# Kernel tuning notes

Hardware: AMD Instinct MI355X
Metric: run time of the kernel (lower is better)

## Reference

```python
import jax, jax.numpy as jnp
import numpy as np

N = 100000          # nodes
D_TEXT = 200        # text embedding dim
D_SEL = 2           # selector embedding dim (zero-padded in pos embs)
D = D_TEXT + D_SEL  # 202
E_TYPES = 6         # 3 forward edge types * 2 (backward edges)
M = 200000          # edges per edge type
N_POS = 512
SMALL_NUMBER = 1e-8


def position_embeddings(n_pos, demb, dpad):
    # Faithful to ProGraML PositionEmbeddings: sinusoid sin||cos, zero-padded.
    pos = jnp.arange(n_pos, dtype=jnp.float32)
    inv_freq = 1.0 / (10000.0 ** (jnp.arange(0, demb, 2, dtype=jnp.float32) / demb))
    sin_inp = pos[:, None] * inv_freq[None, :]                    # [n_pos, demb/2]
    emb = jnp.concatenate([jnp.sin(sin_inp), jnp.cos(sin_inp)], axis=-1)
    return jnp.concatenate([emb, jnp.zeros((n_pos, dpad), emb.dtype)], axis=1)  # [n_pos, demb+dpad]


def setup_inputs() -> dict:
    key = jax.random.key(0)
    ks = jax.random.split(key, 6)
    return {
        "node_states": jax.random.normal(ks[0], (N, D), jnp.float32),
        "edges": jax.random.randint(ks[1], (E_TYPES, M, 2), 0, N),      # [:, :, 0]=src, [:, :, 1]=tgt
        "pos_lists": jax.random.randint(ks[2], (E_TYPES, M), 0, N_POS),
        "W_transform": jax.random.normal(ks[3], (D, D * E_TYPES), jnp.float32) * 0.05,
        "b_transform": jnp.zeros((D * E_TYPES,), jnp.float32),
        "W_pos": jax.random.normal(ks[4], (D, D), jnp.float32) * 0.05,
        "b_pos": jnp.zeros((D,), jnp.float32),
    }


def reference(node_states, edges, pos_lists, W_transform, b_transform, W_pos, b_pos):
    # Positional gating: 2*sigmoid(Linear(position_embs))  -> [512, D]
    pos_embs = position_embeddings(N_POS, D_TEXT, D_SEL)
    pos_gating = 2.0 * jax.nn.sigmoid(pos_embs @ W_pos + b_pos)

    # Dense transform: [N, D] @ [D, E*D] -> view as [N, E, D]
    # (matches torch transpose(0,1).view(E, D, N) followed by per-type transpose back)
    prop = (node_states @ W_transform + b_transform).reshape(N, E_TYPES, D)

    src = edges[..., 0]  # [E, M]
    tgt = edges[..., 1]  # [E, M]

    # Per-edge-type gather of transformed source states: msgs[e, m] = prop[src[e, m], e]
    msgs = prop[src, jnp.arange(E_TYPES)[:, None], :]             # [E, M, D]
    msgs = msgs * pos_gating[pos_lists]                           # positional gate

    # Scatter-add over targets (all edge types fused into one segment_sum)
    flat_tgt = tgt.reshape(-1)
    summed = jax.ops.segment_sum(msgs.reshape(-1, D), flat_tgt, num_segments=N)  # [N, D]

    # Mean aggregation: bincount of targets, zeros treated as 1
    bincount = jax.ops.segment_sum(jnp.ones((E_TYPES * M,), jnp.float32), flat_tgt, num_segments=N)
    divisor = jnp.where(bincount == 0, 1.0, bincount) + SMALL_NUMBER
    return summed / divisor[:, None]
```

## Files before the change

### kernel.cpp

```cpp
#include <hip/hip_runtime.h>
#include <hip/hip_bf16.h>
#include <hip/hip_fp16.h>
#include <math.h>

#define NN   100000
#define NNP  100096
#define DD   202
#define ET   6
#define MM   200000
#define NE   (ET*MM)
#define NPOS 512
#define GDP  204
#define DE   1212
#define PDE  1216
#define KK   202
#define KP   224
#define NP   1280

typedef __attribute__((ext_vector_type(8))) short bf16x8;
typedef __attribute__((ext_vector_type(4))) float f32x4;

static __device__ inline unsigned short f2b(float f) {
    union { __hip_bfloat16 h; unsigned short s; } u;
    u.h = __float2bfloat16(f);
    return u.s;
}

static __device__ inline void glds16(const unsigned short* g, unsigned short* l) {
    __builtin_amdgcn_global_load_lds(
        (const __attribute__((address_space(1))) unsigned int*)g,
        (__attribute__((address_space(3))) unsigned int*)l, 16, 0, 0);
}

__global__ void gating_kernel(const float* __restrict__ W_pos,
                              const float* __restrict__ b_pos,
                              unsigned short* __restrict__ gat) {
    int p = blockIdx.x;
    __shared__ float emb[DD];
    int t = threadIdx.x;
    if (t < 100) {
        float invf = expf(-((float)t / 100.0f) * 9.210340371976184f);
        float si = (float)p * invf;
        emb[t]       = sinf(si);
        emb[100 + t] = cosf(si);
    } else if (t < 102) {
        emb[100 + t] = 0.0f;
    }
    __syncthreads();
    if (t < GDP) {
        float g = 0.0f;
        if (t < DD) {
            float acc = b_pos[t];
            for (int k = 0; k < DD; ++k) acc += emb[k] * W_pos[k * DD + t];
            g = 2.0f / (1.0f + expf(-acc));
        }
        union { __half h; unsigned short s; } u;
        u.h = __float2half_rn(g);
        gat[p * GDP + t] = u.s;
    }
}

__global__ void convB_kernel(const float* __restrict__ W, unsigned short* __restrict__ Bt) {
    int id = blockIdx.x * 256 + threadIdx.x;
    if (id >= NP * KP) return;
    int n = id / KP, k = id % KP;
    float v = (k < KK && n < DE) ? W[(size_t)k * DE + n] : 0.0f;
    Bt[id] = f2b(v);
}

__global__ void convA_kernel(const float* __restrict__ A, unsigned short* __restrict__ Abf) {
    int id = blockIdx.x * 256 + threadIdx.x;
    if (id >= NNP * (KP / 2)) return;
    int row = id / (KP / 2), kp = (id % (KP / 2)) * 2;
    float2 v = make_float2(0.0f, 0.0f);
    if (row < NN && kp < KK) v = *(const float2*)&A[(size_t)row * KK + kp];
    ushort2 o; o.x = f2b(v.x); o.y = f2b(v.y);
    *(ushort2*)&Abf[(size_t)row * KP + kp] = o;
}

__global__ __launch_bounds__(256) void gemm_mfma(const unsigned short* __restrict__ Abf,
                                                 const unsigned short* __restrict__ Bt,
                                                 const float* __restrict__ bias,
                                                 unsigned short* __restrict__ C) {
    __shared__ unsigned short lds[16384];
    unsigned short* sA = lds;
    unsigned short* sB = lds + 8192;
    unsigned short* sE = lds;

    int t    = threadIdx.x;
    int lane = t & 63;
    int wave = t >> 6;
    int q    = lane >> 4;
    int r16  = lane & 15;
    int wm   = (wave >> 1) * 64;
    int wn   = (wave & 1) * 64;
    int row0 = blockIdx.y * 128;
    int col0 = blockIdx.x * 128;

    int lrow = lane >> 2;
    int gch  = (lane & 3) ^ ((lrow >> 1) & 3);
    const unsigned short* aS0 = Abf + (size_t)(row0 + wave * 32 + lrow) * KP + gch * 8;
    const unsigned short* aS1 = aS0 + 16 * KP;
    const unsigned short* bS0 = Bt  + (size_t)(col0 + wave * 32 + lrow) * KP + gch * 8;
    const unsigned short* bS1 = bS0 + 16 * KP;

#define STAGE(b, kc) do {                                   \
        glds16(aS0 + (kc), &sA[(b)*4096 + wave*1024]);      \
        glds16(aS1 + (kc), &sA[(b)*4096 + wave*1024+512]);  \
        glds16(bS0 + (kc), &sB[(b)*4096 + wave*1024]);      \
        glds16(bS1 + (kc), &sB[(b)*4096 + wave*1024+512]);  \
    } while (0)

    f32x4 acc[4][4] = {};
    int swzr = (r16 >> 1) & 3;

    STAGE(0, 0);
    for (int k = 0; k < 7; ++k) {
        int cur = k & 1;
        if (k < 6) {
            STAGE(cur ^ 1, (k + 1) * 32);
            asm volatile("s_waitcnt vmcnt(4)" ::: "memory");
        } else {
            asm volatile("s_waitcnt vmcnt(0)" ::: "memory");
        }
        __builtin_amdgcn_s_barrier();

        bf16x8 a[4], b[4];
        int sbase = cur * 4096;
        #pragma unroll
        for (int mi = 0; mi < 4; ++mi)
            a[mi] = *(const bf16x8*)&sA[sbase + (wm + mi * 16 + r16) * 32 + (q ^ swzr) * 8];
        #pragma unroll
        for (int ni = 0; ni < 4; ++ni)
            b[ni] = *(const bf16x8*)&sB[sbase + (wn + ni * 16 + r16) * 32 + (q ^ swzr) * 8];
        #pragma unroll
        for (int mi = 0; mi < 4; ++mi)
            #pragma unroll
            for (int ni = 0; ni < 4; ++ni)
                acc[mi][ni] = __builtin_amdgcn_mfma_f32_16x16x32_bf16(a[mi], b[ni], acc[mi][ni], 0, 0, 0);

        __builtin_amdgcn_s_barrier();
    }
#undef STAGE

    float bb[4];
    #pragma unroll
    for (int ni = 0; ni < 4; ++ni) {
        int col = col0 + wn + ni * 16 + r16;
        bb[ni] = (col < DE) ? bias[col] : 0.0f;
    }
    int epi = wave * 1152;
    int rl = lane >> 3, ck = lane & 7;
    #pragma unroll
    for (int mi = 0; mi < 4; ++mi) {
        #pragma unroll
        for (int ni = 0; ni < 4; ++ni)
            #pragma unroll
            for (int ri = 0; ri < 4; ++ri)
                sE[epi + (q * 4 + ri) * 72 + ni * 16 + r16] = f2b(acc[mi][ni][ri] + bb[ni]);
        #pragma unroll
        for (int ii = 0; ii < 2; ++ii) {
            int rr = ii * 8 + rl;
            bf16x8 v = *(const bf16x8*)&sE[epi + rr * 72 + ck * 8];
            int grow = row0 + wm + mi * 16 + rr;
            int gcol = col0 + wn + ck * 8;
            if (grow < NN && gcol < PDE)
                *(bf16x8*)&C[(size_t)grow * PDE + gcol] = v;
        }
    }
}

__global__ __launch_bounds__(256) void count_kernel(const int* __restrict__ edges,
                                                    int* __restrict__ count) {
    int i = blockIdx.x * 256 + threadIdx.x;
    if (i >= NE) return;
    atomicAdd(&count[edges[2 * i + 1]], 1);
}

__global__ __launch_bounds__(256) void alloc_kernel(const int* __restrict__ count,
                                                    int* __restrict__ start,
                                                    int* __restrict__ cursor) {
    int t = blockIdx.x * 256 + threadIdx.x;
    int c = (t < NN) ? count[t] : 0;
    __shared__ int s[256];
    __shared__ int base;
    s[threadIdx.x] = c;
    __syncthreads();
    int v = c;
    for (int off = 1; off < 256; off <<= 1) {
        int u = (threadIdx.x >= off) ? s[threadIdx.x - off] : 0;
        __syncthreads();
        v += u;
        s[threadIdx.x] = v;
        __syncthreads();
    }
    if (threadIdx.x == 255) base = atomicAdd(cursor, v);
    __syncthreads();
    if (t < NN) start[t] = base + v - c;
}

__global__ __launch_bounds__(256) void scatter_kernel(const int* __restrict__ edges,
                                                      const int* __restrict__ pos_lists,
                                                      int* __restrict__ start,
                                                      unsigned* __restrict__ recs) {
    int i = blockIdx.x * 256 + threadIdx.x;
    if (i >= NE) return;
    int2 st = *(const int2*)&edges[2 * i];
    int e = (int)((unsigned)i / MM);
    unsigned rec = (unsigned)st.x | ((unsigned)e << 17) | ((unsigned)pos_lists[i] << 20);
    int p = atomicAdd(&start[st.y], 1);
    recs[p] = rec;
}

__global__ __launch_bounds__(256) void gather_kernel(const unsigned short* __restrict__ prop,
                                                     const unsigned short* __restrict__ gat,
                                                     const int* __restrict__ count,
                                                     const int* __restrict__ seg_end,
                                                     const unsigned* __restrict__ recs,
                                                     float* __restrict__ out) {
    int wid = blockIdx.x * 4 + (threadIdx.x >> 6);
    if (wid >= NN) return;
    int lane = threadIdx.x & 63;
    int c = count[wid];
    int end = seg_end[wid];
    int begin = end - c;
    int d = lane * 4;
    bool act = d < DD;
    float a0 = 0.f, a1 = 0.f, a2 = 0.f, a3 = 0.f;

    for (int base = begin; base < end; base += 64) {
        int n = end - base; if (n > 64) n = 64;
        unsigned rec = 0u;
        if (lane < n) rec = recs[base + lane];
        int poff = (int)(rec & 0x1FFFFu) * PDE + (int)((rec >> 17) & 7u) * DD;
        int goff = (int)(rec >> 20) * GDP;

        for (int jj = 0; jj < n; jj += 4) {
            int po[4], go[4];
            #pragma unroll
            for (int u = 0; u < 4; ++u) {
                int j = jj + u; if (j >= n) j = jj;
                po[u] = __shfl(poff, j);
                go[u] = __shfl(goff, j);
            }
            uint2 pv[4], gv[4];
            #pragma unroll
            for (int u = 0; u < 4; ++u) {
                pv[u] = make_uint2(0u, 0u);
                gv[u] = make_uint2(0u, 0u);
                if (act) {
                    pv[u] = *(const uint2*)&prop[po[u] + d];
                    gv[u] = *(const uint2*)&gat[go[u] + d];
                }
            }
            #pragma unroll
            for (int u = 0; u < 4; ++u) {
                if (jj + u < n || u == 0) {
                    float2 g01 = __half22float2(*(const __half2*)&gv[u].x);
                    float2 g23 = __half22float2(*(const __half2*)&gv[u].y);
                    a0 += __uint_as_float(pv[u].x << 16)         * g01.x;
                    a1 += __uint_as_float(pv[u].x & 0xffff0000u) * g01.y;
                    a2 += __uint_as_float(pv[u].y << 16)         * g23.x;
                    a3 += __uint_as_float(pv[u].y & 0xffff0000u) * g23.y;
                }
            }
        }
    }

    float div = (c == 0 ? 1.0f : (float)c) + 1e-8f;
    float inv = 1.0f / div;
    if (act) {
        float* orow = out + (size_t)wid * DD;
        *(float2*)&orow[d] = make_float2(a0 * inv, a1 * inv);
        if (d + 2 < DD) *(float2*)&orow[d + 2] = make_float2(a2 * inv, a3 * inv);
    }
}

extern "C" void kernel_launch(void* const* d_in, const int* in_sizes, int n_in,
                              void* d_out, int out_size, void* d_ws, size_t ws_size,
                              hipStream_t stream) {
    const float* node_states = (const float*)d_in[0];
    const int*   edges       = (const int*)d_in[1];
    const int*   pos_lists   = (const int*)d_in[2];
    const float* W_transform = (const float*)d_in[3];
    const float* b_transform = (const float*)d_in[4];
    const float* W_pos       = (const float*)d_in[5];
    const float* b_pos       = (const float*)d_in[6];
    float* out = (float*)d_out;

    char* ws = (char*)d_ws;
    unsigned short* gat = (unsigned short*)ws;  ws += (size_t)NPOS * GDP * 2;
    int* count  = (int*)ws;                     ws += (size_t)NN * 4;
    int* start  = (int*)ws;                     ws += (size_t)NN * 4;
    int* cursor = (int*)ws;                     ws += 16;
    unsigned short* Bt  = (unsigned short*)ws;  ws += (size_t)NP * KP * 2;
    unsigned short* Abf = (unsigned short*)ws;  ws += (size_t)NNP * KP * 2;
    unsigned* recs = (unsigned*)ws;             ws += (size_t)NE * 4;
    unsigned short* prop = (unsigned short*)ws;

    hipMemsetAsync(count, 0, NN * sizeof(int), stream);
    hipMemsetAsync(cursor, 0, sizeof(int), stream);

    gating_kernel<<<NPOS, 256, 0, stream>>>(W_pos, b_pos, gat);
    convB_kernel<<<(NP * KP + 255) / 256, 256, 0, stream>>>(W_transform, Bt);
    convA_kernel<<<(NNP * (KP / 2) + 255) / 256, 256, 0, stream>>>(node_states, Abf);

    dim3 g2(NP / 128, NNP / 128);
    gemm_mfma<<<g2, 256, 0, stream>>>(Abf, Bt, b_transform, prop);

    count_kernel<<<(NE + 255) / 256, 256, 0, stream>>>(edges, count);
    alloc_kernel<<<(NN + 255) / 256, 256, 0, stream>>>(count, start, cursor);
    scatter_kernel<<<(NE + 255) / 256, 256, 0, stream>>>(edges, pos_lists, start, recs);
    gather_kernel<<<(NN + 3) / 4, 256, 0, stream>>>(prop, gat, count, start, recs, out);
}
```

Baseline: 631.8 us.

## Fuse prep kernels and GEMM with edge scatter into interleaved grids

```diff
diff --git a/kernel.cpp b/kernel.cpp
--- a/kernel.cpp
+++ b/kernel.cpp
@@ -17,6 +17,11 @@
 #define KP   224
 #define NP   1280
 
+#define NB_CONVB 1120
+#define NB_CA    10948
+#define PREPG    1564
+#define MAING    1564
+
 typedef __attribute__((ext_vector_type(8))) short bf16x8;
 typedef __attribute__((ext_vector_type(4))) float f32x4;
 
@@ -32,149 +37,80 @@
         (__attribute__((address_space(3))) unsigned int*)l, 16, 0, 0);
 }
 
-__global__ void gating_kernel(const float* __restrict__ W_pos,
-                              const float* __restrict__ b_pos,
-                              unsigned short* __restrict__ gat) {
-    int p = blockIdx.x;
+__global__ __launch_bounds__(256) void fused_prep(const float* __restrict__ W_pos,
+                                                  const float* __restrict__ b_pos,
+                                                  unsigned short* __restrict__ gat,
+                                                  const float* __restrict__ W,
+                                                  unsigned short* __restrict__ Bt,
+                                                  const float* __restrict__ A,
+                                                  unsigned short* __restrict__ Abf,
+                                                  const int* __restrict__ edges,
+                                                  int* __restrict__ count) {
     __shared__ float emb[DD];
+    int bid = blockIdx.x;
     int t = threadIdx.x;
-    if (t < 100) {
-        float invf = expf(-((float)t / 100.0f) * 9.210340371976184f);
-        float si = (float)p * invf;
-        emb[t]       = sinf(si);
-        emb[100 + t] = cosf(si);
-    } else if (t < 102) {
-        emb[100 + t] = 0.0f;
-    }
-    __syncthreads();
-    if (t < GDP) {
-        float g = 0.0f;
-        if (t < DD) {
-            float acc = b_pos[t];
-            for (int k = 0; k < DD; ++k) acc += emb[k] * W_pos[k * DD + t];
-            g = 2.0f / (1.0f + expf(-acc));
-        }
-        union { __half h; unsigned short s; } u;
-        u.h = __float2half_rn(g);
-        gat[p * GDP + t] = u.s;
-    }
-}
-
-__global__ void convB_kernel(const float* __restrict__ W, unsigned short* __restrict__ Bt) {
-    int id = blockIdx.x * 256 + threadIdx.x;
-    if (id >= NP * KP) return;
-    int n = id / KP, k = id % KP;
-    float v = (k < KK && n < DE) ? W[(size_t)k * DE + n] : 0.0f;
-    Bt[id] = f2b(v);
-}
-
-__global__ void convA_kernel(const float* __restrict__ A, unsigned short* __restrict__ Abf) {
-    int id = blockIdx.x * 256 + threadIdx.x;
-    if (id >= NNP * (KP / 2)) return;
-    int row = id / (KP / 2), kp = (id % (KP / 2)) * 2;
-    float2 v = make_float2(0.0f, 0.0f);
-    if (row < NN && kp < KK) v = *(const float2*)&A[(size_t)row * KK + kp];
-    ushort2 o; o.x = f2b(v.x); o.y = f2b(v.y);
-    *(ushort2*)&Abf[(size_t)row * KP + kp] = o;
-}
-
-__global__ __launch_bounds__(256) void gemm_mfma(const unsigned short* __restrict__ Abf,
-                                                 const unsigned short* __restrict__ Bt,
-                                                 const float* __restrict__ bias,
-                                                 unsigned short* __restrict__ C) {
-    __shared__ unsigned short lds[16384];
-    unsigned short* sA = lds;
-    unsigned short* sB = lds + 8192;
-    unsigned short* sE = lds;
-
-    int t    = threadIdx.x;
-    int lane = t & 63;
-    int wave = t >> 6;
-    int q    = lane >> 4;
-    int r16  = lane & 15;
-    int wm   = (wave >> 1) * 64;
-    int wn   = (wave & 1) * 64;
-    int row0 = blockIdx.y * 128;
-    int col0 = blockIdx.x * 128;
-
-    int lrow = lane >> 2;
-    int gch  = (lane & 3) ^ ((lrow >> 1) & 3);
-    const unsigned short* aS0 = Abf + (size_t)(row0 + wave * 32 + lrow) * KP + gch * 8;
-    const unsigned short* aS1 = aS0 + 16 * KP;
-    const unsigned short* bS0 = Bt  + (size_t)(col0 + wave * 32 + lrow) * KP + gch * 8;
-    const unsigned short* bS1 = bS0 + 16 * KP;
-
-#define STAGE(b, kc) do {                                   \
-        glds16(aS0 + (kc), &sA[(b)*4096 + wave*1024]);      \
-        glds16(aS1 + (kc), &sA[(b)*4096 + wave*1024+512]);  \
-        glds16(bS0 + (kc), &sB[(b)*4096 + wave*1024]);      \
-        glds16(bS1 + (kc), &sB[(b)*4096 + wave*1024+512]);  \
-    } while (0)
-
-    f32x4 acc[4][4] = {};
-    int swzr = (r16 >> 1) & 3;
-
-    STAGE(0, 0);
-    for (int k = 0; k < 7; ++k) {
-        int cur = k & 1;
-        if (k < 6) {
-            STAGE(cur ^ 1, (k + 1) * 32);
-            asm volatile("s_waitcnt vmcnt(4)" ::: "memory");
-        } else {
-            asm volatile("s_waitcnt vmcnt(0)" ::: "memory");
-        }
-        __builtin_amdgcn_s_barrier();
-
-        bf16x8 a[4], b[4];
-        int sbase = cur * 4096;
-        #pragma unroll
-        for (int mi = 0; mi < 4; ++mi)
-            a[mi] = *(const bf16x8*)&sA[sbase + (wm + mi * 16 + r16) * 32 + (q ^ swzr) * 8];
-        #pragma unroll
-        for (int ni = 0; ni < 4; ++ni)
-            b[ni] = *(const bf16x8*)&sB[sbase + (wn + ni * 16 + r16) * 32 + (q ^ swzr) * 8];
-        #pragma unroll
-        for (int mi = 0; mi < 4; ++mi)
-            #pragma unroll
-            for (int ni = 0; ni < 4; ++ni)
-                acc[mi][ni] = __builtin_amdgcn_mfma_f32_16x16x32_bf16(a[mi], b[ni], acc[mi][ni], 0, 0, 0);
-
-        __builtin_amdgcn_s_barrier();
-    }
-#undef STAGE
-
-    float bb[4];
-    #pragma unroll
-    for (int ni = 0; ni < 4; ++ni) {
-        int col = col0 + wn + ni * 16 + r16;
-        bb[ni] = (col < DE) ? bias[col] : 0.0f;
-    }
-    int epi = wave * 1152;
-    int rl = lane >> 3, ck = lane & 7;
-    #pragma unroll
-    for (int mi = 0; mi < 4; ++mi) {
-        #pragma unroll
-        for (int ni = 0; ni < 4; ++ni)
-            #pragma unroll
-            for (int ri = 0; ri < 4; ++ri)
-                sE[epi + (q * 4 + ri) * 72 + ni * 16 + r16] = f2b(acc[mi][ni][ri] + bb[ni]);
-        #pragma unroll
-        for (int ii = 0; ii < 2; ++ii) {
-            int rr = ii * 8 + rl;
-            bf16x8 v = *(const bf16x8*)&sE[epi + rr * 72 + ck * 8];
-            int grow = row0 + wm + mi * 16 + rr;
-            int gcol = col0 + wn + ck * 8;
-            if (grow < NN && gcol < PDE)
-                *(bf16x8*)&C[(size_t)grow * PDE + gcol] = v;
-        }
-    }
-}
-
-__global__ __launch_bounds__(256) void count_kernel(const int* __restrict__ edges,
-                                                    int* __restrict__ count) {
-    int i = blockIdx.x * 256 + threadIdx.x;
-    if (i >= NE) return;
-    atomicAdd(&count[edges[2 * i + 1]], 1);
+
+    if (bid < NPOS) {
+        int p = bid;
+        if (t < 100) {
+            float invf = expf(-((float)t / 100.0f) * 9.210340371976184f);
+            float si = (float)p * invf;
+            emb[t]       = sinf(si);
+            emb[100 + t] = cosf(si);
+        } else if (t < 102) {
+            emb[100 + t] = 0.0f;
+        }
+        __syncthreads();
+        if (t < GDP) {
+            float g = 0.0f;
+            if (t < DD) {
+                float acc = b_pos[t];
+                for (int k = 0; k < DD; ++k) acc += emb[k] * W_pos[k * DD + t];
+                g = 2.0f / (1.0f + expf(-acc));
+            }
+            union { __half h; unsigned short s; } u;
+            u.h = __float2half_rn(g);
+            gat[p * GDP + t] = u.s;
+        }
+        return;
+    }
+    bid -= NPOS;
+
+    if (bid < NB_CONVB) {
+        int id = bid * 256 + t;
+        int n = id / KP, k = id % KP;
+        float v = (k < KK && n < DE) ? W[(size_t)k * DE + n] : 0.0f;
+        Bt[id] = f2b(v);
+        return;
+    }
+    bid -= NB_CONVB;
+
+    int g = bid / 10, s = bid % 10;
+    if (s < 7) {
+        int ca = g * 7 + s;
+        int id = ca * 256 + t;
+        int row = id / 28;
+        int kp  = (id % 28) * 8;
+        bf16x8 o;
+        #pragma unroll
+        for (int j = 0; j < 8; ++j) o[j] = 0;
+        if (row < NN) {
+            const float* ar = A + (size_t)row * KK;
+            #pragma unroll
+            for (int j = 0; j < 4; ++j) {
+                if (kp + 2 * j + 1 < KK) {
+                    float2 v = *(const float2*)&ar[kp + 2 * j];
+                    o[2 * j]     = (short)f2b(v.x);
+                    o[2 * j + 1] = (short)f2b(v.y);
+                }
+            }
+        }
+        *(bf16x8*)&Abf[(size_t)row * KP + kp] = o;
+    } else {
+        int cid = g * 3 + (s - 7);
+        int i = cid * 256 + t;
+        if (i < NE) atomicAdd(&count[edges[2 * i + 1]], 1);
+    }
 }
 
 __global__ __launch_bounds__(256) void alloc_kernel(const int* __restrict__ count,
@@ -199,17 +135,116 @@
     if (t < NN) start[t] = base + v - c;
 }
 
-__global__ __launch_bounds__(256) void scatter_kernel(const int* __restrict__ edges,
-                                                      const int* __restrict__ pos_lists,
-                                                      int* __restrict__ start,
-                                                      unsigned* __restrict__ recs) {
-    int i = blockIdx.x * 256 + threadIdx.x;
-    if (i >= NE) return;
-    int2 st = *(const int2*)&edges[2 * i];
-    int e = (int)((unsigned)i / MM);
-    unsigned rec = (unsigned)st.x | ((unsigned)e << 17) | ((unsigned)pos_lists[i] << 20);
-    int p = atomicAdd(&start[st.y], 1);
-    recs[p] = rec;
+__global__ __launch_bounds__(256) void fused_main(const unsigned short* __restrict__ Abf,
+                                                  const unsigned short* __restrict__ Bt,
+                                                  const float* __restrict__ bias,
+                                                  unsigned short* __restrict__ C,
+                                                  const int* __restrict__ edges,
+                                                  const int* __restrict__ pos_lists,
+                                                  int* __restrict__ start,
+                                                  unsigned* __restrict__ recs) {
+    __shared__ unsigned short lds[16384];
+    int grp = blockIdx.x >> 3, sl = blockIdx.x & 7;
+
+    if (sl >= 5) {
+        int sid = grp * 3 + (sl - 5);
+        int i = sid * 256 + threadIdx.x;
+        if (i < NE) {
+            int2 st = *(const int2*)&edges[2 * i];
+            int e = (int)((unsigned)i / MM);
+            unsigned rec = (unsigned)st.x | ((unsigned)e << 17) | ((unsigned)pos_lists[i] << 20);
+            int p = atomicAdd(&start[st.y], 1);
+            recs[p] = rec;
+        }
+        return;
+    }
+
+    int wg = grp * 5 + sl;
+    unsigned short* sA = lds;
+    unsigned short* sB = lds + 8192;
+    unsigned short* sE = lds;
+
+    int t    = threadIdx.x;
+    int lane = t & 63;
+    int wave = t >> 6;
+    int q    = lane >> 4;
+    int r16  = lane & 15;
+    int wm   = (wave >> 1) * 64;
+    int wn   = (wave & 1) * 64;
+    int row0 = (wg / 10) * 128;
+    int col0 = (wg % 10) * 128;
+
+    int lrow = lane >> 2;
+    int gch  = (lane & 3) ^ ((lrow >> 1) & 3);
+    const unsigned short* aS0 = Abf + (size_t)(row0 + wave * 32 + lrow) * KP + gch * 8;
+    const unsigned short* aS1 = aS0 + 16 * KP;
+    const unsigned short* bS0 = Bt  + (size_t)(col0 + wave * 32 + lrow) * KP + gch * 8;
+    const unsigned short* bS1 = bS0 + 16 * KP;
+
+#define STAGE(b, kc) do {                                   \
+        glds16(aS0 + (kc), &sA[(b)*4096 + wave*1024]);      \
+        glds16(aS1 + (kc), &sA[(b)*4096 + wave*1024+512]);  \
+        glds16(bS0 + (kc), &sB[(b)*4096 + wave*1024]);      \
+        glds16(bS1 + (kc), &sB[(b)*4096 + wave*1024+512]);  \
+    } while (0)
+
+    f32x4 acc[4][4] = {};
+    int swzr = (r16 >> 1) & 3;
+
+    STAGE(0, 0);
+    for (int k = 0; k < 7; ++k) {
+        int cur = k & 1;
+        if (k < 6) {
+            STAGE(cur ^ 1, (k + 1) * 32);
+            asm volatile("s_waitcnt vmcnt(4)" ::: "memory");
+        } else {
+            asm volatile("s_waitcnt vmcnt(0)" ::: "memory");
+        }
+        __builtin_amdgcn_s_barrier();
+
+        bf16x8 a[4], b[4];
+        int sbase = cur * 4096;
+        #pragma unroll
+        for (int mi = 0; mi < 4; ++mi)
+            a[mi] = *(const bf16x8*)&sA[sbase + (wm + mi * 16 + r16) * 32 + (q ^ swzr) * 8];
+        #pragma unroll
+        for (int ni = 0; ni < 4; ++ni)
+            b[ni] = *(const bf16x8*)&sB[sbase + (wn + ni * 16 + r16) * 32 + (q ^ swzr) * 8];
+        #pragma unroll
+        for (int mi = 0; mi < 4; ++mi)
+            #pragma unroll
+            for (int ni = 0; ni < 4; ++ni)
+                acc[mi][ni] = __builtin_amdgcn_mfma_f32_16x16x32_bf16(a[mi], b[ni], acc[mi][ni], 0, 0, 0);
+
+        __builtin_amdgcn_s_barrier();
+    }
+#undef STAGE
+
+    float bb[4];
+    #pragma unroll
+    for (int ni = 0; ni < 4; ++ni) {
+        int col = col0 + wn + ni * 16 + r16;
+        bb[ni] = (col < DE) ? bias[col] : 0.0f;
+    }
+    int epi = wave * 1152;
+    int rl = lane >> 3, ck = lane & 7;
+    #pragma unroll
+    for (int mi = 0; mi < 4; ++mi) {
+        #pragma unroll
+        for (int ni = 0; ni < 4; ++ni)
+            #pragma unroll
+            for (int ri = 0; ri < 4; ++ri)
+                sE[epi + (q * 4 + ri) * 72 + ni * 16 + r16] = f2b(acc[mi][ni][ri] + bb[ni]);
+        #pragma unroll
+        for (int ii = 0; ii < 2; ++ii) {
+            int rr = ii * 8 + rl;
+            bf16x8 v = *(const bf16x8*)&sE[epi + rr * 72 + ck * 8];
+            int grow = row0 + wm + mi * 16 + rr;
+            int gcol = col0 + wn + ck * 8;
+            if (grow < NN && gcol < PDE)
+                *(bf16x8*)&C[(size_t)grow * PDE + gcol] = v;
+        }
+    }
 }
 
 __global__ __launch_bounds__(256) void gather_kernel(const unsigned short* __restrict__ prop,
@@ -301,15 +336,13 @@
     hipMemsetAsync(count, 0, NN * sizeof(int), stream);
     hipMemsetAsync(cursor, 0, sizeof(int), stream);
 
-    gating_kernel<<<NPOS, 256, 0, stream>>>(W_pos, b_pos, gat);
-    convB_kernel<<<(NP * KP + 255) / 256, 256, 0, stream>>>(W_transform, Bt);
-    convA_kernel<<<(NNP * (KP / 2) + 255) / 256, 256, 0, stream>>>(node_states, Abf);
-
-    dim3 g2(NP / 128, NNP / 128);
-    gemm_mfma<<<g2, 256, 0, stream>>>(Abf, Bt, b_transform, prop);
-
-    count_kernel<<<(NE + 255) / 256, 256, 0, stream>>>(edges, count);
+    fused_prep<<<NPOS + NB_CONVB + PREPG * 10, 256, 0, stream>>>(
+        W_pos, b_pos, gat, W_transform, Bt, node_states, Abf, edges, count);
+
     alloc_kernel<<<(NN + 255) / 256, 256, 0, stream>>>(count, start, cursor);
-    scatter_kernel<<<(NE + 255) / 256, 256, 0, stream>>>(edges, pos_lists, start, recs);
+
+    fused_main<<<MAING * 8, 256, 0, stream>>>(
+        Abf, Bt, b_transform, prop, edges, pos_lists, start, recs);
+
     gather_kernel<<<(NN + 3) / 4, 256, 0, stream>>>(prop, gat, count, start, recs, out);
 }
```

Result: faster. 532.7 us (-15.7%).
